# Performance work log

Hardware: AMD Instinct MI355X
Metric: run time of the kernel (lower is better)

Reference implementation:

```python
import jax, jax.numpy as jnp
import numpy as np

STATE_DIM = 256
HID_DIM = 1024
BATCH = 65536
IN_DIM = 2 * STATE_DIM + 1


def setup_inputs() -> dict:
    key = jax.random.key(0)
    ks = jax.random.split(key, 11)
    x0 = jax.random.normal(ks[0], (BATCH, STATE_DIM), dtype=jnp.float32)
    x1 = jax.random.normal(ks[1], (BATCH, STATE_DIM), dtype=jnp.float32)
    t = jax.random.uniform(ks[2], (BATCH, 1), dtype=jnp.float32)

    def linear_init(k, fan_in, fan_out):
        kw, kb = jax.random.split(k)
        bound = 1.0 / np.sqrt(fan_in)
        W = jax.random.uniform(kw, (fan_in, fan_out), minval=-bound, maxval=bound, dtype=jnp.float32)
        b = jax.random.uniform(kb, (fan_out,), minval=-bound, maxval=bound, dtype=jnp.float32)
        return W, b

    W1, b1 = linear_init(ks[3], IN_DIM, HID_DIM)
    W2, b2 = linear_init(ks[4], HID_DIM, HID_DIM)
    W3, b3 = linear_init(ks[5], HID_DIM, HID_DIM)
    W4, b4 = linear_init(ks[6], HID_DIM, STATE_DIM)
    return {"x0": x0, "x1": x1, "t": t,
            "W1": W1, "b1": b1, "W2": W2, "b2": b2,
            "W3": W3, "b3": b3, "W4": W4, "b4": b4}


def _mlp(z, W1, b1, W2, b2, W3, b3, W4, b4):
    h = jax.nn.relu(z @ W1 + b1)
    h = jax.nn.relu(h @ W2 + b2)
    h = jax.nn.relu(h @ W3 + b3)
    return h @ W4 + b4  # [B, state_dim]


def reference(x0, x1, t, W1, b1, W2, b2, W3, b3, W4, b4):
    z = jnp.concatenate((x0, x1, t), axis=1)  # [B, 2*D+1]
    # d(fnn)/dt == last column of the per-sample Jacobian; compute it with one
    # forward-mode JVP using the one-hot tangent on the t slot (fuses with fwd).
    tz = jnp.zeros_like(z).at[:, -1].set(1.0)
    fnn, dt_fnn = jax.jvp(lambda zz: _mlp(zz, W1, b1, W2, b2, W3, b3, W4, b4), (z,), (tz,))
    xt = (1.0 - t) * x0 + t * x1 + t * (1.0 - t) * fnn
    dt_xt = x1 - x0 + (1.0 - t) * fnn - t * fnn + t * (1.0 - t) * dt_fnn
    return (xt, dt_xt)
```

## Files before the change

### kernel.cpp

```cpp
#include <hip/hip_runtime.h>
#include <stdint.h>
#include <stddef.h>


typedef unsigned short u16;
typedef __attribute__((ext_vector_type(8))) short short8;
typedef __attribute__((ext_vector_type(4))) float f32x4;

#define BM 128
#define BN 128
#define BK 64
#define BATCH 65536
#define SDIM 256
#define HDIM 1024

__device__ __forceinline__ u16 f2bf(float f) {
  unsigned int u = __float_as_uint(f);
  u += 0x7FFFu + ((u >> 16) & 1u);
  return (u16)(u >> 16);
}

__device__ __forceinline__ void gload_lds16(const void* g, void* l) {
  __builtin_amdgcn_global_load_lds(
      (const __attribute__((address_space(1))) unsigned int*)g,
      (__attribute__((address_space(3))) unsigned int*)l, 16, 0, 0);
}

struct EpiArgs {
  const float* bias;
  const float* r1;
  const float* t;
  const float* x0;
  const float* x1;
  u16*   out_h;
  u16*   out_u;
  float* out_xt;
  float* out_dt;
};

template <int EPI, bool HASU>
__global__ __launch_bounds__(256, 2)
void fgemm(const u16* __restrict__ Ah, const u16* __restrict__ Au,
           const u16* __restrict__ Bt, int N, int K, EpiArgs e)
{
  __shared__ __align__(16) u16 Ash[BM * BK];
  __shared__ __align__(16) u16 Asu[HASU ? BM * BK : 64];
  __shared__ __align__(16) u16 Bs[BN * BK];

  const int tid  = threadIdx.x;
  const int wave = tid >> 6;
  const int lane = tid & 63;
  const int hi   = lane >> 4;
  const int ln   = lane & 15;

  const int nbx = gridDim.x;
  int bx = blockIdx.x, by = blockIdx.y;
  if ((gridDim.y & 7) == 0) {
    const int id = by * nbx + bx;
    const int g  = id & 7;
    const int s  = id >> 3;
    bx = s % nbx;
    by = (s / nbx) * 8 + g;
  }
  const int bn = bx * BN;
  const int bm = by * BM;

  const int wm = (wave >> 1) * 64;
  const int wn = (wave & 1) * 64;

  f32x4 acch[4][4] = {};
  f32x4 accu[4][4] = {};

  const int srow = lane >> 3;
  const int ssc  = lane & 7;

  for (int k0 = 0; k0 < K; k0 += BK) {
#pragma unroll
    for (int c = 0; c < 4; ++c) {
      const int ch  = wave * 4 + c;
      const int row = ch * 8 + srow;
      const int lc  = ssc ^ (row & 7);
      gload_lds16(Ah + (size_t)(bm + row) * K + k0 + lc * 8, &Ash[ch * 512]);
      gload_lds16(Bt + (size_t)(bn + row) * K + k0 + lc * 8, &Bs[ch * 512]);
      if constexpr (HASU)
        gload_lds16(Au + (size_t)(bm + row) * K + k0 + lc * 8, &Asu[ch * 512]);
    }
    asm volatile("s_waitcnt vmcnt(0)" ::: "memory");
    __syncthreads();

#pragma unroll
    for (int kk = 0; kk < BK; kk += 32) {
      const int sc = ((kk >> 3) + hi) ^ (ln & 7);
      short8 ah[4], au[4], bb[4];
#pragma unroll
      for (int i = 0; i < 4; ++i) {
        const int ro = (wm + i * 16 + ln) * BK + sc * 8;
        ah[i] = *(const short8*)&Ash[ro];
        if constexpr (HASU) au[i] = *(const short8*)&Asu[ro];
      }
#pragma unroll
      for (int i = 0; i < 4; ++i)
        bb[i] = *(const short8*)&Bs[(wn + i * 16 + ln) * BK + sc * 8];
#pragma unroll
      for (int mi = 0; mi < 4; ++mi)
#pragma unroll
        for (int ni = 0; ni < 4; ++ni) {
          acch[mi][ni] = __builtin_amdgcn_mfma_f32_16x16x32_bf16(
              ah[mi], bb[ni], acch[mi][ni], 0, 0, 0);
          if constexpr (HASU)
            accu[mi][ni] = __builtin_amdgcn_mfma_f32_16x16x32_bf16(
                au[mi], bb[ni], accu[mi][ni], 0, 0, 0);
        }
    }
    __syncthreads();
  }

#pragma unroll
  for (int mi = 0; mi < 4; ++mi) {
#pragma unroll
    for (int ni = 0; ni < 4; ++ni) {
      const int n = bn + wn + ni * 16 + ln;
#pragma unroll
      for (int r = 0; r < 4; ++r) {
        const size_t m  = (size_t)(bm + wm + mi * 16 + hi * 4 + r);
        const size_t ix = m * (size_t)N + n;
        const float vh = acch[mi][ni][r];
        if constexpr (EPI == 0) {
          const float r1n = e.r1[n];
          const float pre = vh + e.bias[n] + e.t[m] * r1n;
          e.out_h[ix] = f2bf(fmaxf(pre, 0.f));
          e.out_u[ix] = (pre > 0.f) ? f2bf(r1n) : (u16)0;
        } else if constexpr (EPI == 1) {
          const float vu  = accu[mi][ni][r];
          const float pre = vh + e.bias[n];
          e.out_h[ix] = f2bf(fmaxf(pre, 0.f));
          e.out_u[ix] = (pre > 0.f) ? f2bf(vu) : (u16)0;
        } else {
          const float vu  = accu[mi][ni][r];
          const float fnn = vh + e.bias[n];
          const float tt  = e.t[m];
          const float a   = e.x0[ix];
          const float b   = e.x1[ix];
          const float w   = tt * (1.f - tt);
          e.out_xt[ix] = (1.f - tt) * a + tt * b + w * fnn;
          e.out_dt[ix] = b - a + (1.f - 2.f * tt) * fnn + w * vu;
        }
      }
    }
  }
}

__global__ void prep_z(const float* __restrict__ x0, const float* __restrict__ x1,
                       u16* __restrict__ A0)
{
  const int idx = blockIdx.x * blockDim.x + threadIdx.x;
  const int m = idx >> 7;
  const int c = idx & 127;
  const float* src = (c < 64) ? (x0 + (size_t)m * 256 + c * 4)
                              : (x1 + (size_t)m * 256 + (c - 64) * 4);
  const float4 v = *(const float4*)src;
  uint2 pk;
  pk.x = (unsigned)f2bf(v.x) | ((unsigned)f2bf(v.y) << 16);
  pk.y = (unsigned)f2bf(v.z) | ((unsigned)f2bf(v.w) << 16);
  *(uint2*)&A0[(size_t)m * 512 + c * 4] = pk;
}

__global__ void transpose_cast(const float* __restrict__ W, u16* __restrict__ Wt,
                               int K, int N)
{
  __shared__ float tile[32][33];
  const int tx = threadIdx.x & 31;
  const int ty = threadIdx.x >> 5;
  const int k0 = blockIdx.x * 32;
  const int n0 = blockIdx.y * 32;
#pragma unroll
  for (int i = 0; i < 32; i += 8)
    tile[ty + i][tx] = W[(size_t)(k0 + ty + i) * N + n0 + tx];
  __syncthreads();
#pragma unroll
  for (int i = 0; i < 32; i += 8)
    Wt[(size_t)(n0 + ty + i) * K + k0 + tx] = f2bf(tile[tx][ty + i]);
}

extern "C" void kernel_launch(void* const* d_in, const int* in_sizes, int n_in,
                              void* d_out, int out_size, void* d_ws, size_t ws_size,
                              hipStream_t stream)
{
  const float* x0 = (const float*)d_in[0];
  const float* x1 = (const float*)d_in[1];
  const float* t  = (const float*)d_in[2];
  const float* W1 = (const float*)d_in[3];
  const float* b1 = (const float*)d_in[4];
  const float* W2 = (const float*)d_in[5];
  const float* b2 = (const float*)d_in[6];
  const float* W3 = (const float*)d_in[7];
  const float* b3 = (const float*)d_in[8];
  const float* W4 = (const float*)d_in[9];
  const float* b4 = (const float*)d_in[10];

  char* ws = (char*)d_ws;
  const size_t WB1 = (size_t)512 * HDIM * 2;
  const size_t WB2 = (size_t)HDIM * HDIM * 2;
  const size_t WB4 = (size_t)HDIM * SDIM * 2;
  u16* Wt1 = (u16*)(ws);
  u16* Wt2 = (u16*)(ws + WB1);
  u16* Wt3 = (u16*)(ws + WB1 + WB2);
  u16* Wt4 = (u16*)(ws + WB1 + 2 * WB2);
  const size_t wmark = WB1 + 2 * WB2 + WB4;
  char* act = ws + wmark;

  int nc = 1;
  while (nc < 64 && wmark + (size_t)(BATCH / nc) * 8192 > ws_size) nc <<= 1;
  const int CB = BATCH / nc;

  u16* Ha = (u16*)(act);
  u16* Ua = (u16*)(act + (size_t)CB * 2048);
  u16* Hb = (u16*)(act + (size_t)CB * 4096);
  u16* Ub = (u16*)(act + (size_t)CB * 6144);
  u16* A0c = Hb;

  transpose_cast<<<dim3(16, 32), 256, 0, stream>>>(W1, Wt1, 512, HDIM);
  transpose_cast<<<dim3(32, 32), 256, 0, stream>>>(W2, Wt2, HDIM, HDIM);
  transpose_cast<<<dim3(32, 32), 256, 0, stream>>>(W3, Wt3, HDIM, HDIM);
  transpose_cast<<<dim3(32, 8),  256, 0, stream>>>(W4, Wt4, HDIM, SDIM);

  const float* r1 = W1 + (size_t)512 * HDIM;
  float* out_xt = (float*)d_out;
  float* out_dt = (float*)d_out + (size_t)BATCH * SDIM;

  for (int c = 0; c < nc; ++c) {
    const size_t mb = (size_t)c * CB;
    const dim3 gMid(HDIM / BN, CB / BM);
    const dim3 gOut(SDIM / BN, CB / BM);

    prep_z<<<(CB * 128) / 256, 256, 0, stream>>>(x0 + mb * SDIM, x1 + mb * SDIM, A0c);

    { EpiArgs e{}; e.bias = b1; e.r1 = r1; e.t = t + mb;
      e.out_h = Ha; e.out_u = Ua;
      fgemm<0, false><<<gMid, 256, 0, stream>>>(A0c, nullptr, Wt1, HDIM, 512, e); }

    { EpiArgs e{}; e.bias = b2; e.out_h = Hb; e.out_u = Ub;
      fgemm<1, true><<<gMid, 256, 0, stream>>>(Ha, Ua, Wt2, HDIM, HDIM, e); }

    { EpiArgs e{}; e.bias = b3; e.out_h = Ha; e.out_u = Ua;
      fgemm<1, true><<<gMid, 256, 0, stream>>>(Hb, Ub, Wt3, HDIM, HDIM, e); }

    { EpiArgs e{}; e.bias = b4; e.t = t + mb;
      e.x0 = x0 + mb * SDIM; e.x1 = x1 + mb * SDIM;
      e.out_xt = out_xt + mb * SDIM; e.out_dt = out_dt + mb * SDIM;
      fgemm<2, true><<<gOut, 256, 0, stream>>>(Ha, Ua, Wt4, SDIM, HDIM, e); }
  }
}
```

Before: 1.107 ms.

## Interleave hidden and tangent rows into one stacked GEMM with 256x256 tiles

Stores the activation and its JVP tangent in one buffer, interleaved in blocks of 16 rows. Each layer then runs as a single GEMM with M doubled, so the weight tile in LDS is shared by both streams. The GEMM moves to 512 threads with 256x256 tiles, a double-buffered global-to-LDS prefetch, partial vmcnt waits and s_setprio around the MFMA bursts. This aims to raise MFMA density and cut sync stalls. In exchange it uses 128KB of LDS per block, which may limit occupancy, and the epilogue index remapping is more intricate.

```diff
diff --git a/kernel.cpp b/kernel.cpp
--- a/kernel.cpp
+++ b/kernel.cpp
@@ -7,9 +7,6 @@
 typedef __attribute__((ext_vector_type(8))) short short8;
 typedef __attribute__((ext_vector_type(4))) float f32x4;
 
-#define BM 128
-#define BN 128
-#define BK 64
 #define BATCH 65536
 #define SDIM 256
 #define HDIM 1024
@@ -33,25 +30,25 @@
   const float* x0;
   const float* x1;
   u16*   out_h;
-  u16*   out_u;
   float* out_xt;
   float* out_dt;
 };
 
-template <int EPI, bool HASU>
-__global__ __launch_bounds__(256, 2)
-void fgemm(const u16* __restrict__ Ah, const u16* __restrict__ Au,
-           const u16* __restrict__ Bt, int N, int K, EpiArgs e)
-{
-  __shared__ __align__(16) u16 Ash[BM * BK];
-  __shared__ __align__(16) u16 Asu[HASU ? BM * BK : 64];
-  __shared__ __align__(16) u16 Bs[BN * BK];
+template <int EPI>
+__global__ __launch_bounds__(512, 2)
+void fgemm8(const u16* __restrict__ A, const u16* __restrict__ Bt,
+            int N, int K, EpiArgs e)
+{
+  __shared__ __align__(16) u16 lds[65536];
 
   const int tid  = threadIdx.x;
   const int wave = tid >> 6;
   const int lane = tid & 63;
   const int hi   = lane >> 4;
   const int ln   = lane & 15;
+  const int srow = lane >> 3;
+  const int ssc  = lane & 7;
+  const int lcs  = (ssc ^ srow) * 8;
 
   const int nbx = gridDim.x;
   int bx = blockIdx.x, by = blockIdx.y;
@@ -62,88 +59,134 @@
     bx = s % nbx;
     by = (s / nbx) * 8 + g;
   }
-  const int bn = bx * BN;
-  const int bm = by * BM;
-
-  const int wm = (wave >> 1) * 64;
-  const int wn = (wave & 1) * 64;
-
-  f32x4 acch[4][4] = {};
-  f32x4 accu[4][4] = {};
-
-  const int srow = lane >> 3;
-  const int ssc  = lane & 7;
-
-  for (int k0 = 0; k0 < K; k0 += BK) {
+  const int bn = bx * 256;
+  const int bm = by * 256;
+
+  const int wm = (wave >> 2) * 128;
+  const int wn = (wave & 3) * 64;
+
+  f32x4 acc[8][4] = {};
+
+  const u16* gA = A  + (size_t)bm * K + lcs;
+  const u16* gB = Bt + (size_t)bn * K + lcs;
+  const int NT = K >> 6;
+
+  auto STAGE = [&](int t) {
+    const int kk0 = t << 6;
+    const int lb  = (t & 1) << 15;
 #pragma unroll
     for (int c = 0; c < 4; ++c) {
-      const int ch  = wave * 4 + c;
-      const int row = ch * 8 + srow;
-      const int lc  = ssc ^ (row & 7);
-      gload_lds16(Ah + (size_t)(bm + row) * K + k0 + lc * 8, &Ash[ch * 512]);
-      gload_lds16(Bt + (size_t)(bn + row) * K + k0 + lc * 8, &Bs[ch * 512]);
-      if constexpr (HASU)
-        gload_lds16(Au + (size_t)(bm + row) * K + k0 + lc * 8, &Asu[ch * 512]);
-    }
-    asm volatile("s_waitcnt vmcnt(0)" ::: "memory");
-    __syncthreads();
-
-#pragma unroll
-    for (int kk = 0; kk < BK; kk += 32) {
-      const int sc = ((kk >> 3) + hi) ^ (ln & 7);
-      short8 ah[4], au[4], bb[4];
+      const int ch  = (wave << 2) + c;
+      const int row = (ch << 3) + srow;
+      gload_lds16(gA + (size_t)row * K + kk0, &lds[lb + ch * 512]);
+      gload_lds16(gB + (size_t)row * K + kk0, &lds[lb + 16384 + ch * 512]);
+    }
+  };
+
+  STAGE(0);
+  STAGE(1);
+
+  for (int t = 0; t < NT; ++t) {
+    const int lb = (t & 1) << 15;
+    if (t >= 1 && t + 1 < NT) STAGE(t + 1);
+    if (t + 1 < NT) asm volatile("s_waitcnt vmcnt(8)" ::: "memory");
+    else            asm volatile("s_waitcnt vmcnt(0)" ::: "memory");
+    __builtin_amdgcn_s_barrier();
+
+#pragma unroll
+    for (int p = 0; p < 4; ++p) {
+      const int mbase = (p >> 1) * 4;
+      const int nbase = (p & 1) * 2;
+      short8 ah[4][2], bb[2][2];
 #pragma unroll
       for (int i = 0; i < 4; ++i) {
-        const int ro = (wm + i * 16 + ln) * BK + sc * 8;
-        ah[i] = *(const short8*)&Ash[ro];
-        if constexpr (HASU) au[i] = *(const short8*)&Asu[ro];
-      }
+        const int row = wm + (mbase + i) * 16 + ln;
+#pragma unroll
+        for (int kh = 0; kh < 2; ++kh) {
+          const int scs = (((kh << 2) + hi) ^ (ln & 7)) * 8;
+          ah[i][kh] = *(const short8*)&lds[lb + row * 64 + scs];
+        }
+      }
+#pragma unroll
+      for (int j = 0; j < 2; ++j) {
+        const int row = wn + (nbase + j) * 16 + ln;
+#pragma unroll
+        for (int kh = 0; kh < 2; ++kh) {
+          const int scs = (((kh << 2) + hi) ^ (ln & 7)) * 8;
+          bb[j][kh] = *(const short8*)&lds[lb + 16384 + row * 64 + scs];
+        }
+      }
+      __builtin_amdgcn_s_barrier();
+      asm volatile("s_waitcnt lgkmcnt(0)");
+      __builtin_amdgcn_s_setprio(1);
 #pragma unroll
       for (int i = 0; i < 4; ++i)
-        bb[i] = *(const short8*)&Bs[(wn + i * 16 + ln) * BK + sc * 8];
-#pragma unroll
-      for (int mi = 0; mi < 4; ++mi)
-#pragma unroll
-        for (int ni = 0; ni < 4; ++ni) {
-          acch[mi][ni] = __builtin_amdgcn_mfma_f32_16x16x32_bf16(
-              ah[mi], bb[ni], acch[mi][ni], 0, 0, 0);
-          if constexpr (HASU)
-            accu[mi][ni] = __builtin_amdgcn_mfma_f32_16x16x32_bf16(
-                au[mi], bb[ni], accu[mi][ni], 0, 0, 0);
-        }
-    }
-    __syncthreads();
-  }
-
-#pragma unroll
-  for (int mi = 0; mi < 4; ++mi) {
-#pragma unroll
-    for (int ni = 0; ni < 4; ++ni) {
-      const int n = bn + wn + ni * 16 + ln;
-#pragma unroll
-      for (int r = 0; r < 4; ++r) {
-        const size_t m  = (size_t)(bm + wm + mi * 16 + hi * 4 + r);
-        const size_t ix = m * (size_t)N + n;
-        const float vh = acch[mi][ni][r];
-        if constexpr (EPI == 0) {
-          const float r1n = e.r1[n];
-          const float pre = vh + e.bias[n] + e.t[m] * r1n;
-          e.out_h[ix] = f2bf(fmaxf(pre, 0.f));
-          e.out_u[ix] = (pre > 0.f) ? f2bf(r1n) : (u16)0;
-        } else if constexpr (EPI == 1) {
-          const float vu  = accu[mi][ni][r];
-          const float pre = vh + e.bias[n];
-          e.out_h[ix] = f2bf(fmaxf(pre, 0.f));
-          e.out_u[ix] = (pre > 0.f) ? f2bf(vu) : (u16)0;
-        } else {
-          const float vu  = accu[mi][ni][r];
-          const float fnn = vh + e.bias[n];
+#pragma unroll
+        for (int j = 0; j < 2; ++j) {
+          acc[mbase + i][nbase + j] = __builtin_amdgcn_mfma_f32_16x16x32_bf16(
+              ah[i][0], bb[j][0], acc[mbase + i][nbase + j], 0, 0, 0);
+          acc[mbase + i][nbase + j] = __builtin_amdgcn_mfma_f32_16x16x32_bf16(
+              ah[i][1], bb[j][1], acc[mbase + i][nbase + j], 0, 0, 0);
+        }
+      __builtin_amdgcn_s_setprio(0);
+      __builtin_amdgcn_s_barrier();
+    }
+  }
+
+  if constexpr (EPI == 0) {
+#pragma unroll
+    for (int mi = 0; mi < 8; ++mi) {
+#pragma unroll
+      for (int ni = 0; ni < 4; ++ni) {
+        const int n = bn + wn + ni * 16 + ln;
+        const float bnv = e.bias[n];
+        const float r1n = e.r1[n];
+#pragma unroll
+        for (int r = 0; r < 4; ++r) {
+          const int m = bm + wm + mi * 16 + hi * 4 + r;
+          const float pre = acc[mi][ni][r] + bnv + e.t[m] * r1n;
+          const size_t sH = (size_t)(m >> 4) * 32 + (m & 15);
+          e.out_h[sH * (size_t)N + n]        = f2bf(fmaxf(pre, 0.f));
+          e.out_h[(sH + 16) * (size_t)N + n] = (pre > 0.f) ? f2bf(r1n) : (u16)0;
+        }
+      }
+    }
+  } else if constexpr (EPI == 1) {
+#pragma unroll
+    for (int j = 0; j < 4; ++j) {
+#pragma unroll
+      for (int ni = 0; ni < 4; ++ni) {
+        const int n = bn + wn + ni * 16 + ln;
+        const float bnv = e.bias[n];
+#pragma unroll
+        for (int r = 0; r < 4; ++r) {
+          const size_t sH = (size_t)(bm + wm + j * 32 + hi * 4 + r);
+          const float pre = acc[2 * j][ni][r] + bnv;
+          const float vu  = acc[2 * j + 1][ni][r];
+          e.out_h[sH * (size_t)N + n]        = f2bf(fmaxf(pre, 0.f));
+          e.out_h[(sH + 16) * (size_t)N + n] = (pre > 0.f) ? f2bf(vu) : (u16)0;
+        }
+      }
+    }
+  } else {
+#pragma unroll
+    for (int j = 0; j < 4; ++j) {
+#pragma unroll
+      for (int ni = 0; ni < 4; ++ni) {
+        const int n = bn + wn + ni * 16 + ln;
+        const float bnv = e.bias[n];
+#pragma unroll
+        for (int r = 0; r < 4; ++r) {
+          const int sH = bm + wm + j * 32 + hi * 4 + r;
+          const int m  = ((sH >> 5) << 4) + (hi * 4 + r);
+          const float fnn = acc[2 * j][ni][r] + bnv;
+          const float dtf = acc[2 * j + 1][ni][r];
           const float tt  = e.t[m];
-          const float a   = e.x0[ix];
-          const float b   = e.x1[ix];
-          const float w   = tt * (1.f - tt);
+          const size_t ix = (size_t)m * 256 + n;
+          const float a = e.x0[ix], b = e.x1[ix];
+          const float w = tt * (1.f - tt);
           e.out_xt[ix] = (1.f - tt) * a + tt * b + w * fnn;
-          e.out_dt[ix] = b - a + (1.f - 2.f * tt) * fnn + w * vu;
+          e.out_dt[ix] = b - a + (1.f - 2.f * tt) * fnn + w * dtf;
         }
       }
     }
@@ -213,11 +256,9 @@
   while (nc < 64 && wmark + (size_t)(BATCH / nc) * 8192 > ws_size) nc <<= 1;
   const int CB = BATCH / nc;
 
-  u16* Ha = (u16*)(act);
-  u16* Ua = (u16*)(act + (size_t)CB * 2048);
-  u16* Hb = (u16*)(act + (size_t)CB * 4096);
-  u16* Ub = (u16*)(act + (size_t)CB * 6144);
-  u16* A0c = Hb;
+  u16* Sa = (u16*)(act);
+  u16* Sb = (u16*)(act + (size_t)CB * 4096);
+  u16* Zc = Sb;
 
   transpose_cast<<<dim3(16, 32), 256, 0, stream>>>(W1, Wt1, 512, HDIM);
   transpose_cast<<<dim3(32, 32), 256, 0, stream>>>(W2, Wt2, HDIM, HDIM);
@@ -230,24 +271,21 @@
 
   for (int c = 0; c < nc; ++c) {
     const size_t mb = (size_t)c * CB;
-    const dim3 gMid(HDIM / BN, CB / BM);
-    const dim3 gOut(SDIM / BN, CB / BM);
-
-    prep_z<<<(CB * 128) / 256, 256, 0, stream>>>(x0 + mb * SDIM, x1 + mb * SDIM, A0c);
-
-    { EpiArgs e{}; e.bias = b1; e.r1 = r1; e.t = t + mb;
-      e.out_h = Ha; e.out_u = Ua;
-      fgemm<0, false><<<gMid, 256, 0, stream>>>(A0c, nullptr, Wt1, HDIM, 512, e); }
-
-    { EpiArgs e{}; e.bias = b2; e.out_h = Hb; e.out_u = Ub;
-      fgemm<1, true><<<gMid, 256, 0, stream>>>(Ha, Ua, Wt2, HDIM, HDIM, e); }
-
-    { EpiArgs e{}; e.bias = b3; e.out_h = Ha; e.out_u = Ua;
-      fgemm<1, true><<<gMid, 256, 0, stream>>>(Hb, Ub, Wt3, HDIM, HDIM, e); }
+
+    prep_z<<<(CB * 128) / 256, 256, 0, stream>>>(x0 + mb * SDIM, x1 + mb * SDIM, Zc);
+
+    { EpiArgs e{}; e.bias = b1; e.r1 = r1; e.t = t + mb; e.out_h = Sa;
+      fgemm8<0><<<dim3(HDIM / 256, CB / 256), 512, 0, stream>>>(Zc, Wt1, HDIM, 512, e); }
+
+    { EpiArgs e{}; e.bias = b2; e.out_h = Sb;
+      fgemm8<1><<<dim3(HDIM / 256, CB / 128), 512, 0, stream>>>(Sa, Wt2, HDIM, HDIM, e); }
+
+    { EpiArgs e{}; e.bias = b3; e.out_h = Sa;
+      fgemm8<1><<<dim3(HDIM / 256, CB / 128), 512, 0, stream>>>(Sb, Wt3, HDIM, HDIM, e); }
 
     { EpiArgs e{}; e.bias = b4; e.t = t + mb;
       e.x0 = x0 + mb * SDIM; e.x1 = x1 + mb * SDIM;
       e.out_xt = out_xt + mb * SDIM; e.out_dt = out_dt + mb * SDIM;
-      fgemm<2, true><<<gOut, 256, 0, stream>>>(Ha, Ua, Wt4, SDIM, HDIM, e); }
-  }
-}
+      fgemm8<2><<<dim3(SDIM / 256, CB / 128), 512, 0, stream>>>(Sa, Wt4, SDIM, HDIM, e); }
+  }
+}
```

Measured after the change: 1.238 ms. +11.8%, slower.
